# Kernel tuning notes

Hardware: AMD Instinct MI355X
Metric: run time of the kernel (lower is better)

## Reference

```python
import jax, jax.numpy as jnp
import numpy as np

B, N, D_IN, D_OUT, MAX_POS = 256, 256, 768, 300, 256
NEG_INF = -9e15
LEAKY_SLOPE = 0.2


def setup_inputs() -> dict:
    key = jax.random.key(0)
    ks = jax.random.split(key, 6)
    h = jax.random.normal(ks[0], (B, N, D_IN), dtype=jnp.float32)
    adj = (jax.random.uniform(ks[1], (B, N, N)) > 0.9).astype(jnp.float32)
    adj = jnp.maximum(adj, jnp.eye(N, dtype=jnp.float32)[None])
    positions = jax.random.randint(ks[2], (B, N), 0, MAX_POS)
    W = jax.random.normal(ks[3], (D_IN, D_OUT), dtype=jnp.float32) * (1.0 / np.sqrt(D_IN))
    a_src = jax.random.normal(ks[4], (1, D_OUT), dtype=jnp.float32) * 0.05
    a_dst = jax.random.normal(ks[5], (1, D_OUT), dtype=jnp.float32) * 0.05
    pos_table = jax.random.normal(jax.random.fold_in(key, 7), (MAX_POS, D_OUT), dtype=jnp.float32)
    return {"h": h, "adj": adj, "positions": positions, "W": W,
            "a_src": a_src, "a_dst": a_dst, "pos_table": pos_table}


def reference(h, adj, positions, W, a_src, a_dst, pos_table):
    # Wh = W(h) + position embedding          [B, N, D_OUT]
    Wh = jnp.einsum('bni,io->bno', h, W) + pos_table[positions]
    # additive attention scores
    f_src = jnp.einsum('bno,o->bn', Wh, a_src[0])  # [B, N]
    f_dst = jnp.einsum('bno,o->bn', Wh, a_dst[0])  # [B, N]
    e = f_src[:, :, None] + f_dst[:, None, :]      # [B, N, N]
    e = jnp.where(e >= 0, e, LEAKY_SLOPE * e)      # LeakyReLU(0.2)
    # adjacency masking + softmax over last dim
    masked = jnp.where(adj > 0, e, NEG_INF)
    attention = jax.nn.softmax(masked, axis=-1)
    # (eval mode: edge dropout and dropout are identity)
    h_prime = jnp.einsum('bnm,bmo->bno', attention, Wh)
    return h_prime, attention
```

## Files before the change

### kernel.cpp

```cpp
#include <hip/hip_runtime.h>

#define B_    256
#define N_    256
#define DIN   768
#define DOUT  300
#define DOUTP 320
#define M_    (B_*N_)
#define HP_ELEMS (M_*DOUT)
#define NEG_INF -9.0e15f

typedef _Float16 f16;
typedef __attribute__((ext_vector_type(8))) _Float16 f16x8;
typedef __attribute__((ext_vector_type(4))) _Float16 f16x4;
typedef __attribute__((ext_vector_type(4))) float    f32x4;

__global__ __launch_bounds__(256) void prep_wt(const float* __restrict__ W,
                                               f16* __restrict__ WtT) {
    int idx = blockIdx.x * 256 + threadIdx.x;
    if (idx >= DIN * DOUTP) return;
    int k = idx / DOUTP, n = idx - k * DOUTP;
    float v = (n < DOUT) ? W[k * DOUT + n] : 0.0f;
    WtT[(((size_t)(k >> 5) * DOUTP + n) << 5) + (k & 31)] = (f16)v;
}

__global__ __launch_bounds__(256, 2) void gemm1(
    const float* __restrict__ h, const f16* __restrict__ WtT,
    const int* __restrict__ positions,
    const float* __restrict__ a_src, const float* __restrict__ a_dst,
    const float* __restrict__ pos_table,
    f16* __restrict__ WhT2, float* __restrict__ f_src, float* __restrict__ f_dst)
{
    __shared__ float pfs[64][4], pfd[64][4];

    const int tid  = threadIdx.x;
    const int wave = tid >> 6, lane = tid & 63;
    const int quad = lane >> 4, c = lane & 15;
    const int rowbase = blockIdx.x * 64;

    const float* ab0 = h + (size_t)(rowbase + c) * DIN + quad * 8;
    const float* ab1 = ab0 + 16 * DIN;
    const float* ab2 = ab0 + 32 * DIN;
    const float* ab3 = ab0 + 48 * DIN;

    int boffs[5];
#pragma unroll
    for (int i = 0; i < 5; ++i) {
        int n = (wave * 5 + i) * 16 + c;
        boffs[i] = (n << 5) + (quad << 3);
    }

    f32x4 acc[4][5];
#pragma unroll
    for (int rt = 0; rt < 4; ++rt)
#pragma unroll
        for (int i = 0; i < 5; ++i) acc[rt][i] = (f32x4){0.f, 0.f, 0.f, 0.f};

    float4 av[2][4][2];
    f16x8  bs[2][5];
    f16x8  af[4];

#define LOADA(KT, S) do {                                                      \
    av[S][0][0] = *(const float4*)(ab0 + (KT) * 32);                           \
    av[S][0][1] = *(const float4*)(ab0 + (KT) * 32 + 4);                       \
    av[S][1][0] = *(const float4*)(ab1 + (KT) * 32);                           \
    av[S][1][1] = *(const float4*)(ab1 + (KT) * 32 + 4);                       \
    av[S][2][0] = *(const float4*)(ab2 + (KT) * 32);                           \
    av[S][2][1] = *(const float4*)(ab2 + (KT) * 32 + 4);                       \
    av[S][3][0] = *(const float4*)(ab3 + (KT) * 32);                           \
    av[S][3][1] = *(const float4*)(ab3 + (KT) * 32 + 4);                       \
} while (0)

#define LOADB(KT, S) do {                                                      \
    const f16* p_ = WtT + (size_t)(KT) * (DOUTP * 32);                         \
    _Pragma("unroll")                                                          \
    for (int i_ = 0; i_ < 5; ++i_)                                             \
        bs[S][i_] = *(const f16x8*)(p_ + boffs[i_]);                           \
} while (0)

#define CVT(S) do {                                                            \
    _Pragma("unroll")                                                          \
    for (int rt_ = 0; rt_ < 4; ++rt_) {                                        \
        float4 u0 = av[S][rt_][0], u1 = av[S][rt_][1];                         \
        af[rt_] = (f16x8){(f16)u0.x, (f16)u0.y, (f16)u0.z, (f16)u0.w,          \
                          (f16)u1.x, (f16)u1.y, (f16)u1.z, (f16)u1.w};         \
    } } while (0)

#define COMP(S) do {                                                           \
    __builtin_amdgcn_s_setprio(1);                                             \
    _Pragma("unroll")                                                          \
    for (int rt_ = 0; rt_ < 4; ++rt_)                                          \
        _Pragma("unroll")                                                      \
        for (int i_ = 0; i_ < 5; ++i_)                                         \
            acc[rt_][i_] = __builtin_amdgcn_mfma_f32_16x16x32_f16(             \
                af[rt_], bs[S][i_], acc[rt_][i_], 0, 0, 0);                    \
    __builtin_amdgcn_s_setprio(0);                                             \
} while (0)

    LOADA(0, 0);
    LOADB(0, 0);
#pragma unroll
    for (int kt = 0; kt < 24; ++kt) {
        if (kt + 1 < 24) {
            LOADA(kt + 1, (kt + 1) & 1);
            LOADB(kt + 1, (kt + 1) & 1);
        }
        CVT(kt & 1);
        COMP(kt & 1);
    }
#undef COMP
#undef CVT
#undef LOADB
#undef LOADA

    const int bidx = rowbase >> 8;
    const int ktb0 = (rowbase & 255) >> 5;

    int posr[4][4];
#pragma unroll
    for (int rt = 0; rt < 4; ++rt)
#pragma unroll
        for (int r = 0; r < 4; ++r)
            posr[rt][r] = positions[rowbase + rt * 16 + quad * 4 + r];

    float fs[4][4], fd[4][4];
#pragma unroll
    for (int rt = 0; rt < 4; ++rt)
#pragma unroll
        for (int r = 0; r < 4; ++r) { fs[rt][r] = 0.f; fd[rt][r] = 0.f; }

#pragma unroll
    for (int i = 0; i < 5; ++i) {
        int col = (wave * 5 + i) * 16 + c;
        if (col < DOUT) {
            float as = a_src[col], ad = a_dst[col];
#pragma unroll
            for (int rt = 0; rt < 4; ++rt)
#pragma unroll
                for (int r = 0; r < 4; ++r) {
                    float v = acc[rt][i][r] + pos_table[posr[rt][r] * DOUT + col];
                    acc[rt][i][r] = v;
                    fs[rt][r] += v * as;
                    fd[rt][r] += v * ad;
                }
        } else {
#pragma unroll
            for (int rt = 0; rt < 4; ++rt)
#pragma unroll
                for (int r = 0; r < 4; ++r) acc[rt][i][r] = 0.0f;
        }
    }
#pragma unroll
    for (int off = 1; off < 16; off <<= 1) {
#pragma unroll
        for (int rt = 0; rt < 4; ++rt)
#pragma unroll
            for (int r = 0; r < 4; ++r) {
                fs[rt][r] += __shfl_xor(fs[rt][r], off, 16);
                fd[rt][r] += __shfl_xor(fd[rt][r], off, 16);
            }
    }
    if (c == 0) {
#pragma unroll
        for (int rt = 0; rt < 4; ++rt)
#pragma unroll
            for (int r = 0; r < 4; ++r) {
                int row = rt * 16 + quad * 4 + r;
                pfs[row][wave] = fs[rt][r];
                pfd[row][wave] = fd[rt][r];
            }
    }
#pragma unroll
    for (int i = 0; i < 5; ++i) {
        int col = (wave * 5 + i) * 16 + c;
#pragma unroll
        for (int rt = 0; rt < 4; ++rt) {
            f16x4 u = (f16x4){(f16)acc[rt][i][0], (f16)acc[rt][i][1],
                              (f16)acc[rt][i][2], (f16)acc[rt][i][3]};
            size_t off = (((size_t)(bidx * 8 + ktb0 + (rt >> 1)) * 8
                           + (rt & 1) * 4 + quad) * DOUTP + col) * 4;
            *(f16x4*)(WhT2 + off) = u;
        }
    }
    __syncthreads();
    if (tid < 64) {
        f_src[rowbase + tid] = pfs[tid][0] + pfs[tid][1] + pfs[tid][2] + pfs[tid][3];
        f_dst[rowbase + tid] = pfd[tid][0] + pfd[tid][1] + pfd[tid][2] + pfd[tid][3];
    }
}

__global__ __launch_bounds__(256, 3) void fused2(
    const float* __restrict__ adj, const float* __restrict__ f_src,
    const float* __restrict__ f_dst, const f16* __restrict__ WhT2,
    float* __restrict__ att, float* __restrict__ hp)
{
    __shared__ f16 Pl[64 * 256];

    const int tid  = threadIdx.x;
    const int wave = tid >> 6, lane = tid & 63;
    const int quad = lane >> 4, c = lane & 15;
    const int rowbase = blockIdx.x * 64;
    const int bidx = rowbase >> 8;
    const int cx7 = c & 7;

    const f16* wbase = WhT2 + (size_t)bidx * 8 * (DOUTP * 32);

    f16x8 bs[2][5];
#define PREF2(KT, S) do {                                                      \
    const f16* p_ = wbase + (size_t)(KT) * (DOUTP * 32);                       \
    _Pragma("unroll")                                                          \
    for (int i_ = 0; i_ < 5; ++i_) {                                           \
        int n_ = (wave * 5 + i_) * 16 + c;                                     \
        f16x4 lo_ = *(const f16x4*)(p_ + (2 * quad) * (DOUTP * 4) + n_ * 4);   \
        f16x4 hi_ = *(const f16x4*)(p_ + (2 * quad + 1) * (DOUTP * 4) + n_ * 4); \
        bs[S][i_] = (f16x8){lo_[0], lo_[1], lo_[2], lo_[3],                    \
                            hi_[0], hi_[1], hi_[2], hi_[3]};                   \
    } } while (0)

    {
        float4 fd4 = *(const float4*)(f_dst + bidx * N_ + lane * 4);
        const float* arow = adj + (size_t)(rowbase + wave * 16) * N_ + lane * 4;
        float4 nx0 = *(const float4*)arow;
        float4 nx1 = *(const float4*)(arow + N_);
        for (int rr = 0; rr < 16; ++rr) {
            float4 a4 = nx0;
            nx0 = nx1;
            if (rr + 2 < 16) nx1 = *(const float4*)(arow + (size_t)(rr + 2) * N_);
            const int lrow = wave * 16 + rr;
            const int row  = rowbase + lrow;
            float fsv = f_src[row];

            float v, e0, e1, e2, e3;
            v = fsv + fd4.x; v = v >= 0.f ? v : 0.2f * v; e0 = a4.x > 0.f ? v : NEG_INF;
            v = fsv + fd4.y; v = v >= 0.f ? v : 0.2f * v; e1 = a4.y > 0.f ? v : NEG_INF;
            v = fsv + fd4.z; v = v >= 0.f ? v : 0.2f * v; e2 = a4.z > 0.f ? v : NEG_INF;
            v = fsv + fd4.w; v = v >= 0.f ? v : 0.2f * v; e3 = a4.w > 0.f ? v : NEG_INF;

            float mx = fmaxf(fmaxf(e0, e1), fmaxf(e2, e3));
#pragma unroll
            for (int off = 1; off < 64; off <<= 1) mx = fmaxf(mx, __shfl_xor(mx, off, 64));

            float p0 = __expf(e0 - mx), p1 = __expf(e1 - mx);
            float p2 = __expf(e2 - mx), p3 = __expf(e3 - mx);
            float s = p0 + p1 + p2 + p3;
#pragma unroll
            for (int off = 1; off < 64; off <<= 1) s += __shfl_xor(s, off, 64);

            float inv = 1.0f / s;
            *(float4*)(att + (size_t)row * N_ + lane * 4) =
                make_float4(p0 * inv, p1 * inv, p2 * inv, p3 * inv);
            int slot = (lane >> 1) ^ (lrow & 7);
            *(f16x4*)&Pl[lrow * 256 + slot * 8 + (lane & 1) * 4] =
                (f16x4){(f16)(p0 * inv), (f16)(p1 * inv), (f16)(p2 * inv), (f16)(p3 * inv)};
        }
    }
    PREF2(0, 0);
    __syncthreads();

    f32x4 acc[4][5];
#pragma unroll
    for (int rt = 0; rt < 4; ++rt)
#pragma unroll
        for (int i = 0; i < 5; ++i) acc[rt][i] = (f32x4){0.f, 0.f, 0.f, 0.f};

#define COMPUTE2(KT, S) do {                                                   \
    const int k4_ = (KT) * 4 + quad;                                           \
    __builtin_amdgcn_s_setprio(1);                                             \
    _Pragma("unroll")                                                          \
    for (int rt_ = 0; rt_ < 4; ++rt_) {                                        \
        f16x8 af = *(const f16x8*)&Pl[(rt_ * 16 + c) * 256 + ((k4_ ^ cx7) << 3)]; \
        _Pragma("unroll")                                                      \
        for (int i_ = 0; i_ < 5; ++i_)                                         \
            acc[rt_][i_] = __builtin_amdgcn_mfma_f32_16x16x32_f16(             \
                af, bs[S][i_], acc[rt_][i_], 0, 0, 0);                         \
    }                                                                          \
    __builtin_amdgcn_s_setprio(0);                                             \
    } while (0)

#pragma unroll
    for (int kt2 = 0; kt2 < 4; ++kt2) {
        const int ktA = 2 * kt2, ktB = 2 * kt2 + 1;
        PREF2(ktB, 1);
        COMPUTE2(ktA, 0);
        if (ktB + 1 < 8) PREF2(ktB + 1, 0);
        COMPUTE2(ktB, 1);
    }
#undef COMPUTE2
#undef PREF2

#pragma unroll
    for (int i = 0; i < 5; ++i) {
        int col = (wave * 5 + i) * 16 + c;
        if (col < DOUT) {
#pragma unroll
            for (int rt = 0; rt < 4; ++rt) {
                int row0 = rowbase + rt * 16 + quad * 4;
#pragma unroll
                for (int r = 0; r < 4; ++r)
                    hp[(size_t)(row0 + r) * DOUT + col] = acc[rt][i][r];
            }
        }
    }
}

extern "C" void kernel_launch(void* const* d_in, const int* in_sizes, int n_in,
                              void* d_out, int out_size, void* d_ws, size_t ws_size,
                              hipStream_t stream)
{
    const float* h         = (const float*)d_in[0];
    const float* adj       = (const float*)d_in[1];
    const int*   positions = (const int*)d_in[2];
    const float* W         = (const float*)d_in[3];
    const float* a_src     = (const float*)d_in[4];
    const float* a_dst     = (const float*)d_in[5];
    const float* pos_table = (const float*)d_in[6];

    float* hp  = (float*)d_out;
    float* att = hp + HP_ELEMS;

    f16*   WtT   = (f16*)d_ws;
    f16*   WhT2  = WtT + (size_t)DOUTP * DIN;
    float* f_src = (float*)(WhT2 + (size_t)B_ * DOUTP * N_);
    float* f_dst = f_src + M_;

    hipLaunchKernelGGL(prep_wt, dim3((DIN * DOUTP + 255) / 256), dim3(256), 0, stream, W, WtT);
    hipLaunchKernelGGL(gemm1,   dim3(M_ / 64), dim3(256), 0, stream,
                       h, WtT, positions, a_src, a_dst, pos_table, WhT2, f_src, f_dst);
    hipLaunchKernelGGL(fused2,  dim3(M_ / 64), dim3(256), 0, stream,
                       adj, f_src, f_dst, WhT2, att, hp);
}
```

Baseline: 486.5 us.

## Split gemm1 into single-wave blocks per column group with partial score sums

```diff
diff --git a/kernel.cpp b/kernel.cpp
--- a/kernel.cpp
+++ b/kernel.cpp
@@ -20,32 +20,38 @@
     if (idx >= DIN * DOUTP) return;
     int k = idx / DOUTP, n = idx - k * DOUTP;
     float v = (n < DOUT) ? W[k * DOUT + n] : 0.0f;
-    WtT[(((size_t)(k >> 5) * DOUTP + n) << 5) + (k & 31)] = (f16)v;
+    int p = k & 31;
+    int slot = (p < 16) ? ((p >> 2) * 8 + (p & 3))
+                        : (((p - 16) >> 2) * 8 + 4 + ((p - 16) & 3));
+    WtT[(((size_t)(k >> 5) * DOUTP + n) << 5) + slot] = (f16)v;
 }
 
-__global__ __launch_bounds__(256, 2) void gemm1(
+__global__ __launch_bounds__(64) void gemm1(
     const float* __restrict__ h, const f16* __restrict__ WtT,
     const int* __restrict__ positions,
     const float* __restrict__ a_src, const float* __restrict__ a_dst,
     const float* __restrict__ pos_table,
-    f16* __restrict__ WhT2, float* __restrict__ f_src, float* __restrict__ f_dst)
+    f16* __restrict__ WhT2, float* __restrict__ f_srcP, float* __restrict__ f_dstP)
 {
-    __shared__ float pfs[64][4], pfd[64][4];
-
-    const int tid  = threadIdx.x;
-    const int wave = tid >> 6, lane = tid & 63;
+    const int lane = threadIdx.x;
     const int quad = lane >> 4, c = lane & 15;
-    const int rowbase = blockIdx.x * 64;
-
-    const float* ab0 = h + (size_t)(rowbase + c) * DIN + quad * 8;
-    const float* ab1 = ab0 + 16 * DIN;
-    const float* ab2 = ab0 + 32 * DIN;
-    const float* ab3 = ab0 + 48 * DIN;
+
+    const int d = blockIdx.x;
+    const int work  = (d & 7) * 512 + (d >> 3);
+    const int strip = work >> 2;
+    const int cg    = work & 3;
+    const int rowbase = strip * 64;
+    const int colbase = cg * 80;
+
+    const float* a0 = h + (size_t)(rowbase + c) * DIN + quad * 4;
+    const float* a1 = a0 + 16 * DIN;
+    const float* a2 = a0 + 32 * DIN;
+    const float* a3 = a0 + 48 * DIN;
 
     int boffs[5];
 #pragma unroll
     for (int i = 0; i < 5; ++i) {
-        int n = (wave * 5 + i) * 16 + c;
+        int n = colbase + i * 16 + c;
         boffs[i] = (n << 5) + (quad << 3);
     }
 
@@ -56,18 +62,18 @@
         for (int i = 0; i < 5; ++i) acc[rt][i] = (f32x4){0.f, 0.f, 0.f, 0.f};
 
     float4 av[2][4][2];
-    f16x8  bs[2][5];
+    f16x8  bs[3][5];
     f16x8  af[4];
 
 #define LOADA(KT, S) do {                                                      \
-    av[S][0][0] = *(const float4*)(ab0 + (KT) * 32);                           \
-    av[S][0][1] = *(const float4*)(ab0 + (KT) * 32 + 4);                       \
-    av[S][1][0] = *(const float4*)(ab1 + (KT) * 32);                           \
-    av[S][1][1] = *(const float4*)(ab1 + (KT) * 32 + 4);                       \
-    av[S][2][0] = *(const float4*)(ab2 + (KT) * 32);                           \
-    av[S][2][1] = *(const float4*)(ab2 + (KT) * 32 + 4);                       \
-    av[S][3][0] = *(const float4*)(ab3 + (KT) * 32);                           \
-    av[S][3][1] = *(const float4*)(ab3 + (KT) * 32 + 4);                       \
+    av[S][0][0] = *(const float4*)(a0 + (KT) * 32);                            \
+    av[S][0][1] = *(const float4*)(a0 + (KT) * 32 + 16);                       \
+    av[S][1][0] = *(const float4*)(a1 + (KT) * 32);                            \
+    av[S][1][1] = *(const float4*)(a1 + (KT) * 32 + 16);                       \
+    av[S][2][0] = *(const float4*)(a2 + (KT) * 32);                            \
+    av[S][2][1] = *(const float4*)(a2 + (KT) * 32 + 16);                       \
+    av[S][3][0] = *(const float4*)(a3 + (KT) * 32);                            \
+    av[S][3][1] = *(const float4*)(a3 + (KT) * 32 + 16);                       \
 } while (0)
 
 #define LOADB(KT, S) do {                                                      \
@@ -98,14 +104,13 @@
 
     LOADA(0, 0);
     LOADB(0, 0);
+    LOADB(1, 1);
 #pragma unroll
     for (int kt = 0; kt < 24; ++kt) {
-        if (kt + 1 < 24) {
-            LOADA(kt + 1, (kt + 1) & 1);
-            LOADB(kt + 1, (kt + 1) & 1);
-        }
+        if (kt + 1 < 24) LOADA(kt + 1, (kt + 1) & 1);
+        if (kt + 2 < 24) LOADB(kt + 2, (kt + 2) % 3);
         CVT(kt & 1);
-        COMP(kt & 1);
+        COMP(kt % 3);
     }
 #undef COMP
 #undef CVT
@@ -130,7 +135,7 @@
 
 #pragma unroll
     for (int i = 0; i < 5; ++i) {
-        int col = (wave * 5 + i) * 16 + c;
+        int col = colbase + i * 16 + c;
         if (col < DOUT) {
             float as = a_src[col], ad = a_dst[col];
 #pragma unroll
@@ -164,14 +169,14 @@
         for (int rt = 0; rt < 4; ++rt)
 #pragma unroll
             for (int r = 0; r < 4; ++r) {
-                int row = rt * 16 + quad * 4 + r;
-                pfs[row][wave] = fs[rt][r];
-                pfd[row][wave] = fd[rt][r];
+                int row = rowbase + rt * 16 + quad * 4 + r;
+                f_srcP[(size_t)cg * M_ + row] = fs[rt][r];
+                f_dstP[(size_t)cg * M_ + row] = fd[rt][r];
             }
     }
 #pragma unroll
     for (int i = 0; i < 5; ++i) {
-        int col = (wave * 5 + i) * 16 + c;
+        int col = colbase + i * 16 + c;
 #pragma unroll
         for (int rt = 0; rt < 4; ++rt) {
             f16x4 u = (f16x4){(f16)acc[rt][i][0], (f16)acc[rt][i][1],
@@ -181,16 +186,11 @@
             *(f16x4*)(WhT2 + off) = u;
         }
     }
-    __syncthreads();
-    if (tid < 64) {
-        f_src[rowbase + tid] = pfs[tid][0] + pfs[tid][1] + pfs[tid][2] + pfs[tid][3];
-        f_dst[rowbase + tid] = pfd[tid][0] + pfd[tid][1] + pfd[tid][2] + pfd[tid][3];
-    }
 }
 
 __global__ __launch_bounds__(256, 3) void fused2(
-    const float* __restrict__ adj, const float* __restrict__ f_src,
-    const float* __restrict__ f_dst, const f16* __restrict__ WhT2,
+    const float* __restrict__ adj, const float* __restrict__ f_srcP,
+    const float* __restrict__ f_dstP, const f16* __restrict__ WhT2,
     float* __restrict__ att, float* __restrict__ hp)
 {
     __shared__ f16 Pl[64 * 256];
@@ -217,7 +217,14 @@
     } } while (0)
 
     {
-        float4 fd4 = *(const float4*)(f_dst + bidx * N_ + lane * 4);
+        float4 q0 = *(const float4*)(f_dstP + (size_t)bidx * N_ + lane * 4);
+        float4 q1 = *(const float4*)(f_dstP + M_ + (size_t)bidx * N_ + lane * 4);
+        float4 q2 = *(const float4*)(f_dstP + 2 * (size_t)M_ + (size_t)bidx * N_ + lane * 4);
+        float4 q3 = *(const float4*)(f_dstP + 3 * (size_t)M_ + (size_t)bidx * N_ + lane * 4);
+        float4 fd4 = make_float4(q0.x + q1.x + q2.x + q3.x,
+                                 q0.y + q1.y + q2.y + q3.y,
+                                 q0.z + q1.z + q2.z + q3.z,
+                                 q0.w + q1.w + q2.w + q3.w);
         const float* arow = adj + (size_t)(rowbase + wave * 16) * N_ + lane * 4;
         float4 nx0 = *(const float4*)arow;
         float4 nx1 = *(const float4*)(arow + N_);
@@ -227,7 +234,8 @@
             if (rr + 2 < 16) nx1 = *(const float4*)(arow + (size_t)(rr + 2) * N_);
             const int lrow = wave * 16 + rr;
             const int row  = rowbase + lrow;
-            float fsv = f_src[row];
+            float fsv = f_srcP[row] + f_srcP[M_ + row]
+                      + f_srcP[2 * (size_t)M_ + row] + f_srcP[3 * (size_t)M_ + row];
 
             float v, e0, e1, e2, e3;
             v = fsv + fd4.x; v = v >= 0.f ? v : 0.2f * v; e0 = a4.x > 0.f ? v : NEG_INF;
@@ -317,14 +325,14 @@
     float* hp  = (float*)d_out;
     float* att = hp + HP_ELEMS;
 
-    f16*   WtT   = (f16*)d_ws;
-    f16*   WhT2  = WtT + (size_t)DOUTP * DIN;
-    float* f_src = (float*)(WhT2 + (size_t)B_ * DOUTP * N_);
-    float* f_dst = f_src + M_;
+    f16*   WtT    = (f16*)d_ws;
+    f16*   WhT2   = WtT + (size_t)DOUTP * DIN;
+    float* f_srcP = (float*)(WhT2 + (size_t)B_ * DOUTP * N_);
+    float* f_dstP = f_srcP + 4 * (size_t)M_;
 
     hipLaunchKernelGGL(prep_wt, dim3((DIN * DOUTP + 255) / 256), dim3(256), 0, stream, W, WtT);
-    hipLaunchKernelGGL(gemm1,   dim3(M_ / 64), dim3(256), 0, stream,
-                       h, WtT, positions, a_src, a_dst, pos_table, WhT2, f_src, f_dst);
+    hipLaunchKernelGGL(gemm1,   dim3(4096), dim3(64), 0, stream,
+                       h, WtT, positions, a_src, a_dst, pos_table, WhT2, f_srcP, f_dstP);
     hipLaunchKernelGGL(fused2,  dim3(M_ / 64), dim3(256), 0, stream,
-                       adj, f_src, f_dst, WhT2, att, hp);
+                       adj, f_srcP, f_dstP, WhT2, att, hp);
 }
```

Result: slower. 529.2 us (+8.8%).

## Stage W tiles into LDS via async global_load_lds with triple buffering

Applied to the files above, without the earlier changes.

```diff
diff --git a/kernel.cpp b/kernel.cpp
--- a/kernel.cpp
+++ b/kernel.cpp
@@ -14,13 +14,20 @@
 typedef __attribute__((ext_vector_type(4))) _Float16 f16x4;
 typedef __attribute__((ext_vector_type(4))) float    f32x4;
 
+__device__ __forceinline__ void async_copy16(void* lds, const void* g) {
+    __builtin_amdgcn_global_load_lds(
+        (const __attribute__((address_space(1))) void*)g,
+        (__attribute__((address_space(3))) void*)lds, 16, 0, 0);
+}
+
 __global__ __launch_bounds__(256) void prep_wt(const float* __restrict__ W,
                                                f16* __restrict__ WtT) {
     int idx = blockIdx.x * 256 + threadIdx.x;
     if (idx >= DIN * DOUTP) return;
     int k = idx / DOUTP, n = idx - k * DOUTP;
     float v = (n < DOUT) ? W[k * DOUT + n] : 0.0f;
-    WtT[(((size_t)(k >> 5) * DOUTP + n) << 5) + (k & 31)] = (f16)v;
+    int kt = k >> 5, sl = ((k >> 3) & 3) ^ ((n >> 1) & 3), e = k & 7;
+    WtT[(((size_t)kt * DOUTP + n) << 5) + (sl << 3) + e] = (f16)v;
 }
 
 __global__ __launch_bounds__(256, 2) void gemm1(
@@ -30,6 +37,7 @@
     const float* __restrict__ pos_table,
     f16* __restrict__ WhT2, float* __restrict__ f_src, float* __restrict__ f_dst)
 {
+    __shared__ f16 Bs[3][DOUTP * 32];
     __shared__ float pfs[64][4], pfd[64][4];
 
     const int tid  = threadIdx.x;
@@ -37,16 +45,16 @@
     const int quad = lane >> 4, c = lane & 15;
     const int rowbase = blockIdx.x * 64;
 
-    const float* ab0 = h + (size_t)(rowbase + c) * DIN + quad * 8;
-    const float* ab1 = ab0 + 16 * DIN;
-    const float* ab2 = ab0 + 32 * DIN;
-    const float* ab3 = ab0 + 48 * DIN;
+    const float* a0 = h + (size_t)(rowbase + c) * DIN + quad * 8;
+    const float* a1 = a0 + 16 * DIN;
+    const float* a2 = a0 + 32 * DIN;
+    const float* a3 = a0 + 48 * DIN;
 
     int boffs[5];
 #pragma unroll
     for (int i = 0; i < 5; ++i) {
         int n = (wave * 5 + i) * 16 + c;
-        boffs[i] = (n << 5) + (quad << 3);
+        boffs[i] = (n << 5) + ((quad ^ ((n >> 1) & 3)) << 3);
     }
 
     f32x4 acc[4][5];
@@ -56,25 +64,26 @@
         for (int i = 0; i < 5; ++i) acc[rt][i] = (f32x4){0.f, 0.f, 0.f, 0.f};
 
     float4 av[2][4][2];
-    f16x8  bs[2][5];
     f16x8  af[4];
 
+#define STAGEB(KT, BUF) do {                                                   \
+    _Pragma("unroll")                                                          \
+    for (int i_ = 0; i_ < 5; ++i_) {                                           \
+        int chk_ = wave * 5 + i_;                                              \
+        async_copy16((char*)Bs[BUF] + chk_ * 1024,                             \
+                     (const char*)WtT + (size_t)(KT) * 20480 + chk_ * 1024     \
+                                      + lane * 16);                            \
+    } } while (0)
+
 #define LOADA(KT, S) do {                                                      \
-    av[S][0][0] = *(const float4*)(ab0 + (KT) * 32);                           \
-    av[S][0][1] = *(const float4*)(ab0 + (KT) * 32 + 4);                       \
-    av[S][1][0] = *(const float4*)(ab1 + (KT) * 32);                           \
-    av[S][1][1] = *(const float4*)(ab1 + (KT) * 32 + 4);                       \
-    av[S][2][0] = *(const float4*)(ab2 + (KT) * 32);                           \
-    av[S][2][1] = *(const float4*)(ab2 + (KT) * 32 + 4);                       \
-    av[S][3][0] = *(const float4*)(ab3 + (KT) * 32);                           \
-    av[S][3][1] = *(const float4*)(ab3 + (KT) * 32 + 4);                       \
-} while (0)
-
-#define LOADB(KT, S) do {                                                      \
-    const f16* p_ = WtT + (size_t)(KT) * (DOUTP * 32);                         \
-    _Pragma("unroll")                                                          \
-    for (int i_ = 0; i_ < 5; ++i_)                                             \
-        bs[S][i_] = *(const f16x8*)(p_ + boffs[i_]);                           \
+    av[S][0][0] = *(const float4*)(a0 + (KT) * 32);                            \
+    av[S][0][1] = *(const float4*)(a0 + (KT) * 32 + 4);                        \
+    av[S][1][0] = *(const float4*)(a1 + (KT) * 32);                            \
+    av[S][1][1] = *(const float4*)(a1 + (KT) * 32 + 4);                        \
+    av[S][2][0] = *(const float4*)(a2 + (KT) * 32);                            \
+    av[S][2][1] = *(const float4*)(a2 + (KT) * 32 + 4);                        \
+    av[S][3][0] = *(const float4*)(a3 + (KT) * 32);                            \
+    av[S][3][1] = *(const float4*)(a3 + (KT) * 32 + 4);                        \
 } while (0)
 
 #define CVT(S) do {                                                            \
@@ -85,32 +94,66 @@
                           (f16)u1.x, (f16)u1.y, (f16)u1.z, (f16)u1.w};         \
     } } while (0)
 
-#define COMP(S) do {                                                           \
+#define ITER(KT, SA, SB, PA, PB, VM) do {                                      \
+    asm volatile("s_waitcnt vmcnt(" #VM ")");                                  \
+    __builtin_amdgcn_sched_barrier(0);                                         \
+    __builtin_amdgcn_s_barrier();                                              \
+    __builtin_amdgcn_sched_barrier(0);                                         \
+    CVT(SA);                                                                   \
     __builtin_amdgcn_s_setprio(1);                                             \
     _Pragma("unroll")                                                          \
-    for (int rt_ = 0; rt_ < 4; ++rt_)                                          \
-        _Pragma("unroll")                                                      \
-        for (int i_ = 0; i_ < 5; ++i_)                                         \
-            acc[rt_][i_] = __builtin_amdgcn_mfma_f32_16x16x32_f16(             \
-                af[rt_], bs[S][i_], acc[rt_][i_], 0, 0, 0);                    \
+    for (int i_ = 0; i_ < 5; ++i_) {                                           \
+        f16x8 bf = *(const f16x8*)&Bs[SB][boffs[i_]];                          \
+        acc[0][i_] = __builtin_amdgcn_mfma_f32_16x16x32_f16(af[0], bf, acc[0][i_], 0, 0, 0); \
+        acc[1][i_] = __builtin_amdgcn_mfma_f32_16x16x32_f16(af[1], bf, acc[1][i_], 0, 0, 0); \
+        acc[2][i_] = __builtin_amdgcn_mfma_f32_16x16x32_f16(af[2], bf, acc[2][i_], 0, 0, 0); \
+        acc[3][i_] = __builtin_amdgcn_mfma_f32_16x16x32_f16(af[3], bf, acc[3][i_], 0, 0, 0); \
+    }                                                                          \
     __builtin_amdgcn_s_setprio(0);                                             \
+    __builtin_amdgcn_sched_barrier(0);                                         \
+    __builtin_amdgcn_s_barrier();                                              \
+    __builtin_amdgcn_sched_barrier(0);                                         \
+    if (PA) { LOADA((KT) + 2, SA); }                                           \
+    __builtin_amdgcn_sched_barrier(0);                                         \
+    if (PB) { STAGEB((KT) + 3, SB); }                                          \
+    __builtin_amdgcn_sched_barrier(0);                                         \
 } while (0)
 
-    LOADA(0, 0);
-    LOADB(0, 0);
-#pragma unroll
-    for (int kt = 0; kt < 24; ++kt) {
-        if (kt + 1 < 24) {
-            LOADA(kt + 1, (kt + 1) & 1);
-            LOADB(kt + 1, (kt + 1) & 1);
-        }
-        CVT(kt & 1);
-        COMP(kt & 1);
-    }
-#undef COMP
+    LOADA(0, 0);  __builtin_amdgcn_sched_barrier(0);
+    STAGEB(0, 0); __builtin_amdgcn_sched_barrier(0);
+    LOADA(1, 1);  __builtin_amdgcn_sched_barrier(0);
+    STAGEB(1, 1); __builtin_amdgcn_sched_barrier(0);
+    STAGEB(2, 2); __builtin_amdgcn_sched_barrier(0);
+
+    ITER( 0, 0, 0, 1, 1, 18);
+    ITER( 1, 1, 1, 1, 1, 18);
+    ITER( 2, 0, 2, 1, 1, 18);
+    ITER( 3, 1, 0, 1, 1, 18);
+    ITER( 4, 0, 1, 1, 1, 18);
+    ITER( 5, 1, 2, 1, 1, 18);
+    ITER( 6, 0, 0, 1, 1, 18);
+    ITER( 7, 1, 1, 1, 1, 18);
+    ITER( 8, 0, 2, 1, 1, 18);
+    ITER( 9, 1, 0, 1, 1, 18);
+    ITER(10, 0, 1, 1, 1, 18);
+    ITER(11, 1, 2, 1, 1, 18);
+    ITER(12, 0, 0, 1, 1, 18);
+    ITER(13, 1, 1, 1, 1, 18);
+    ITER(14, 0, 2, 1, 1, 18);
+    ITER(15, 1, 0, 1, 1, 18);
+    ITER(16, 0, 1, 1, 1, 18);
+    ITER(17, 1, 2, 1, 1, 18);
+    ITER(18, 0, 0, 1, 1, 18);
+    ITER(19, 1, 1, 1, 1, 18);
+    ITER(20, 0, 2, 1, 1, 18);
+    ITER(21, 1, 0, 1, 0, 18);
+    ITER(22, 0, 1, 0, 0, 13);
+    ITER(23, 1, 2, 0, 0,  0);
+
+#undef ITER
 #undef CVT
-#undef LOADB
 #undef LOADA
+#undef STAGEB
 
     const int bidx = rowbase >> 8;
     const int ktb0 = (rowbase & 255) >> 5;
```

Measured after the change: 489.9 us. About the same (+0.7%).
